# Optimization experiments

Hardware: AMD Instinct MI355X
Metric: run time of the kernel (lower is better)

## Reference

```python
import jax, jax.numpy as jnp
import numpy as np

N, E = 50000, 800000
D_IN_N, D_IN_E, D_OUT = 64, 64, 64


def setup_inputs() -> dict:
    key = jax.random.key(0)
    ks = jax.random.split(key, 10)
    stdv = 1.0 / np.sqrt(D_OUT)
    u = lambda k, shape: jax.random.uniform(k, shape, jnp.float32, -stdv, stdv)
    return {
        "nf": jax.random.normal(ks[0], (N, D_IN_N), jnp.float32),
        "ef": jax.random.normal(ks[1], (E, D_IN_E), jnp.float32),
        "src": jax.random.randint(ks[2], (E,), 0, N, jnp.int32),
        "dst": jax.random.randint(ks[3], (E,), 0, N, jnp.int32),
        "W_node": u(ks[4], (D_IN_N, D_OUT)),
        "W_edge": u(ks[5], (D_IN_E, D_OUT)),
        "bias_node": u(ks[6], (D_OUT,)),
        "bias_edge": u(ks[7], (D_OUT,)),
        "W_dense": u(ks[8], (2 * D_OUT, D_OUT)),  # Linear(2*out, out) weight, stored transposed
        "b_dense": u(ks[9], (D_OUT,)),
    }


def reference(nf, ef, src, dst, W_node, W_edge, bias_node, bias_edge, W_dense, b_dense):
    n_nodes = nf.shape[0]
    # input projections
    nf_h = nf @ W_node                     # [N, D]
    ef_h = ef @ W_edge                     # [E, D]
    # update_all: mean of incoming edge features per dst node (0 for isolated nodes, DGL default)
    deg = jax.ops.segment_sum(jnp.ones((ef_h.shape[0],), ef_h.dtype), dst, num_segments=n_nodes)
    nb_ef = jax.ops.segment_sum(ef_h, dst, num_segments=n_nodes) / jnp.maximum(deg, 1.0)[:, None]
    # apply_nodes: nf = act(nf + bias)
    nf_out = jax.nn.relu(nf_h + bias_node)
    # apply_edges (uses updated nf): cat([ef + nb_ef[dst], (nf[src]+nf[dst])/2]) -> Linear -> +bias -> act
    tmp_ef = ef_h + nb_ef[dst]             # [E, D]
    srcdst_nf = (nf_out[src] + nf_out[dst]) * 0.5
    ef_out = jnp.concatenate([tmp_ef, srcdst_nf], axis=1) @ W_dense + b_dense + bias_edge
    ef_out = jax.nn.relu(ef_out)
    return nf_out, ef_out
```

## Files before the change

### kernel.cpp

```cpp
#include <hip/hip_runtime.h>

#define D 64

typedef __attribute__((ext_vector_type(8))) short short8;
typedef __attribute__((ext_vector_type(4))) float f32x4;

__device__ __forceinline__ ushort f2b(float f) {
    union { float f; unsigned u; } x; x.f = f;
    unsigned r = x.u + 0x7FFFu + ((x.u >> 16) & 1u);
    return (ushort)(r >> 16);
}
__device__ __forceinline__ float b2f(ushort u) {
    union { float f; unsigned u; } x; x.u = ((unsigned)u) << 16;
    return x.f;
}
__device__ __forceinline__ short8 pack8(float4 a, float4 b) {
    short8 r;
    r[0] = (short)f2b(a.x); r[1] = (short)f2b(a.y); r[2] = (short)f2b(a.z); r[3] = (short)f2b(a.w);
    r[4] = (short)f2b(b.x); r[5] = (short)f2b(b.y); r[6] = (short)f2b(b.z); r[7] = (short)f2b(b.w);
    return r;
}

__global__ __launch_bounds__(256) void setup_kernel(
    const float* __restrict__ W_edge, const float* __restrict__ W_dense,
    const float* __restrict__ b_dense, const float* __restrict__ bias_edge,
    ushort* __restrict__ Wcomb_b, float* __restrict__ bias2)
{
    const int tid = threadIdx.x;
    for (int idx = tid; idx < D * D; idx += 256) {
        int k = idx >> 6, n = idx & 63;
        float s = 0.f;
        #pragma unroll 8
        for (int j = 0; j < D; ++j)
            s = fmaf(W_edge[k * D + j], W_dense[j * D + n], s);
        Wcomb_b[n * D + k] = f2b(s);
    }
    if (tid < D) bias2[tid] = b_dense[tid] + bias_edge[tid];
}

__global__ __launch_bounds__(256) void node_proj_kernel(
    const float* __restrict__ nf, const float* __restrict__ Wn,
    const float* __restrict__ bias, const float* __restrict__ Wd_bot,
    float* __restrict__ out, ushort* __restrict__ nfp_b, int N)
{
    constexpr int ROWS = 16;
    __shared__ float Ws[D * D];
    __shared__ float Wb[D * D];
    __shared__ float As[ROWS * D];
    __shared__ float Vs[ROWS * D];
    const int tid = threadIdx.x;
    const long row0 = (long)blockIdx.x * ROWS;

    #pragma unroll
    for (int i = tid; i < D * D / 4; i += 256) {
        ((float4*)Ws)[i] = ((const float4*)Wn)[i];
        float4 v = ((const float4*)Wd_bot)[i];
        ((float4*)Wb)[i] = make_float4(0.5f * v.x, 0.5f * v.y, 0.5f * v.z, 0.5f * v.w);
    }
    {
        int i = tid;
        long r = row0 + (i * 4) / D;
        ((float4*)As)[i] = (r < N) ? ((const float4*)nf)[row0 * D / 4 + i]
                                   : make_float4(0.f, 0.f, 0.f, 0.f);
    }
    __syncthreads();

    const int c = tid & 63;
    const float b = bias[c];
    for (int rr = tid >> 6; rr < ROWS; rr += 4) {
        float acc = 0.f;
        #pragma unroll
        for (int k = 0; k < D; ++k)
            acc = fmaf(As[rr * D + k], Ws[k * D + c], acc);
        float v = fmaxf(acc + b, 0.f);
        Vs[rr * D + c] = v;
        long r = row0 + rr;
        if (r < N) out[r * D + c] = v;
    }
    __syncthreads();
    for (int rr = tid >> 6; rr < ROWS; rr += 4) {
        float acc = 0.f;
        #pragma unroll
        for (int k = 0; k < D; ++k)
            acc = fmaf(Vs[rr * D + k], Wb[k * D + c], acc);
        long r = row0 + rr;
        if (r < N) nfp_b[r * D + c] = f2b(acc);
    }
}

__global__ __launch_bounds__(256) void hist_kernel(
    const int* __restrict__ dst, int* __restrict__ deg_i, int E)
{
    int i = blockIdx.x * 256 + threadIdx.x;
    if (i < E) atomicAdd(deg_i + dst[i], 1);
}

__global__ __launch_bounds__(256) void scanA_kernel(
    const int* __restrict__ deg_i, int* __restrict__ pos,
    int* __restrict__ bsum, int N)
{
    __shared__ int s[256];
    const int tid = threadIdx.x;
    const int i = blockIdx.x * 256 + tid;
    int v = (i < N) ? deg_i[i] : 0;
    s[tid] = v;
    __syncthreads();
    #pragma unroll
    for (int off = 1; off < 256; off <<= 1) {
        int t = (tid >= off) ? s[tid - off] : 0;
        __syncthreads();
        s[tid] += t;
        __syncthreads();
    }
    if (i < N) pos[i] = s[tid] - v;
    if (tid == 255) bsum[blockIdx.x] = s[255];
}

__global__ __launch_bounds__(256) void scanB_kernel(int* __restrict__ bsum, int NB)
{
    __shared__ int s[256];
    const int tid = threadIdx.x;
    int v = (tid < NB) ? bsum[tid] : 0;
    s[tid] = v;
    __syncthreads();
    #pragma unroll
    for (int off = 1; off < 256; off <<= 1) {
        int t = (tid >= off) ? s[tid - off] : 0;
        __syncthreads();
        s[tid] += t;
        __syncthreads();
    }
    if (tid < NB) bsum[tid] = s[tid] - v;
}

__global__ __launch_bounds__(256) void scanC_kernel(
    int* __restrict__ pos, int* __restrict__ cursor,
    const int* __restrict__ bsum, int N)
{
    int i = blockIdx.x * 256 + threadIdx.x;
    if (i < N) {
        int p = pos[i] + bsum[blockIdx.x];
        pos[i] = p;
        cursor[i] = p;
    }
}

__global__ __launch_bounds__(256) void scatter_kernel(
    const int* __restrict__ dst, int* __restrict__ cursor,
    int2* __restrict__ sorted_ed, int E)
{
    int i = blockIdx.x * 256 + threadIdx.x;
    if (i < E) {
        int dv = dst[i];
        int slot = atomicAdd(cursor + dv, 1);
        sorted_ed[slot] = make_int2(i, dv);
    }
}

#define SEG_ROWS 128
__global__ __launch_bounds__(256) void efp_seg_kernel(
    const float* __restrict__ ef, const int2* __restrict__ sorted_ed,
    const ushort* __restrict__ Wt, ushort* __restrict__ efp,
    float* __restrict__ nb_sum, int E)
{
    __shared__ float Sf[SEG_ROWS * 68];
    __shared__ int eids[SEG_ROWS];
    __shared__ int dsts[SEG_ROWS];
    const int tid = threadIdx.x;
    const long s0 = (long)blockIdx.x * SEG_ROWS;

    if (tid < SEG_ROWS) {
        long s = s0 + tid;
        int2 p2 = (s < E) ? sorted_ed[s] : make_int2(0, -1);
        eids[tid] = p2.x;
        dsts[tid] = p2.y;
    }
    __syncthreads();

    const int w = tid >> 6, lane = tid & 63;
    const int lr = lane & 15, g = lane >> 4;

    float4 va[2][4];
    #pragma unroll
    for (int tt = 0; tt < 2; ++tt) {
        const long erow = eids[64 * tt + 16 * w + lr];
        const float4* ap = (const float4*)(ef + erow * D);
        va[tt][0] = ap[2 * g];     va[tt][1] = ap[2 * g + 1];
        va[tt][2] = ap[8 + 2 * g]; va[tt][3] = ap[8 + 2 * g + 1];
    }

    short8 bf0[4], bf1[4];
    #pragma unroll
    for (int t = 0; t < 4; ++t) {
        bf0[t] = *(const short8*)&Wt[(16 * t + lr) * D + 8 * g];
        bf1[t] = *(const short8*)&Wt[(16 * t + lr) * D + 32 + 8 * g];
    }

    #pragma unroll
    for (int tt = 0; tt < 2; ++tt) {
        short8 a0 = pack8(va[tt][0], va[tt][1]);
        short8 a1 = pack8(va[tt][2], va[tt][3]);
        f32x4 acc[4];
        #pragma unroll
        for (int t = 0; t < 4; ++t) {
            f32x4 z = {0.f, 0.f, 0.f, 0.f};
            z = __builtin_amdgcn_mfma_f32_16x16x32_bf16(a0, bf0[t], z, 0, 0, 0);
            z = __builtin_amdgcn_mfma_f32_16x16x32_bf16(a1, bf1[t], z, 0, 0, 0);
            acc[t] = z;
        }

        #pragma unroll
        for (int t = 0; t < 4; ++t) {
            int c = 16 * t + lr;
            #pragma unroll
            for (int reg = 0; reg < 4; ++reg)
                Sf[(64 * tt + 16 * w + 4 * g + reg) * 68 + c] = acc[t][reg];
        }

        const bool odd = lane & 1;
        const int rb = 64 * tt + 16 * w + 4 * g + (odd ? 2 : 0);
        long sl0 = s0 + rb, sl1 = s0 + rb + 1;
        long eo0 = (long)eids[rb] * D, eo1 = (long)eids[rb + 1] * D;
        #pragma unroll
        for (int t = 0; t < 4; ++t) {
            float p0 = __shfl_xor(acc[t][0], 1, 64);
            float p1 = __shfl_xor(acc[t][1], 1, 64);
            float p2 = __shfl_xor(acc[t][2], 1, 64);
            float p3 = __shfl_xor(acc[t][3], 1, 64);
            float lo0, hi0, lo1, hi1;
            if (odd) { lo0 = p2; hi0 = acc[t][2]; lo1 = p3; hi1 = acc[t][3]; }
            else     { lo0 = acc[t][0]; hi0 = p0; lo1 = acc[t][1]; hi1 = p1; }
            int cbase = 16 * t + (lr & ~1);
            unsigned dw0 = ((unsigned)f2b(hi0) << 16) | (unsigned)f2b(lo0);
            unsigned dw1 = ((unsigned)f2b(hi1) << 16) | (unsigned)f2b(lo1);
            if (sl0 < E) *(unsigned*)(efp + eo0 + cbase) = dw0;
            if (sl1 < E) *(unsigned*)(efp + eo1 + cbase) = dw1;
        }
    }
    __syncthreads();

    {
        const int col = tid & 63;
        const int r0 = (tid >> 6) * 32;
        float seg = 0.f;
        int cur = dsts[r0];
        #pragma unroll 4
        for (int r = r0; r < r0 + 32; ++r) {
            int dv = dsts[r];
            if (dv != cur) {
                if (cur >= 0) atomicAdd(nb_sum + (long)cur * D + col, seg);
                seg = 0.f;
                cur = dv;
            }
            seg += Sf[r * 68 + col];
        }
        if (cur >= 0) atomicAdd(nb_sum + (long)cur * D + col, seg);
    }
}

__global__ __launch_bounds__(256) void ndp_lite_kernel(
    const float* __restrict__ nb_sum, const int* __restrict__ deg_i,
    const ushort* __restrict__ nfp_b, ushort* __restrict__ ndp_b, int N)
{
    long i = (long)blockIdx.x * 256 + threadIdx.x;
    long node = i >> 3;
    int cb = (int)(i & 7);
    if (node >= N) return;
    float inv = 1.0f / fmaxf((float)deg_i[node], 1.0f);
    const float4* sp = (const float4*)(nb_sum + node * D + cb * 8);
    float4 x0 = sp[0], x1 = sp[1];
    short8 np = *(const short8*)(nfp_b + node * D + cb * 8);
    short8 r;
    r[0] = (short)f2b(x0.x * inv + b2f((ushort)np[0]));
    r[1] = (short)f2b(x0.y * inv + b2f((ushort)np[1]));
    r[2] = (short)f2b(x0.z * inv + b2f((ushort)np[2]));
    r[3] = (short)f2b(x0.w * inv + b2f((ushort)np[3]));
    r[4] = (short)f2b(x1.x * inv + b2f((ushort)np[4]));
    r[5] = (short)f2b(x1.y * inv + b2f((ushort)np[5]));
    r[6] = (short)f2b(x1.z * inv + b2f((ushort)np[6]));
    r[7] = (short)f2b(x1.w * inv + b2f((ushort)np[7]));
    *(short8*)(ndp_b + node * D + cb * 8) = r;
}

__global__ __launch_bounds__(256) void final_kernel(
    const ushort* __restrict__ efp, const int* __restrict__ src,
    const int* __restrict__ dst, const ushort* __restrict__ ndp_b,
    const ushort* __restrict__ nfp_b, const float* __restrict__ bias2,
    float* __restrict__ out, int E)
{
    long idx = (long)blockIdx.x * 256 + threadIdx.x;
    long e = idx >> 2;
    int q = (int)(idx & 3);
    if (e >= E) return;
    int dv = dst[e], sv = src[e];
    const short8* ep = (const short8*)(efp + e * D + q * 16);
    const short8* np = (const short8*)(ndp_b + (long)dv * D + q * 16);
    const short8* sp = (const short8*)(nfp_b + (long)sv * D + q * 16);
    short8 e0 = ep[0], e1 = ep[1];
    short8 n0 = np[0], n1 = np[1];
    short8 s0 = sp[0], s1 = sp[1];
    const float4* bp = (const float4*)(bias2 + q * 16);
    float4 b0 = bp[0], b1 = bp[1], b2 = bp[2], b3 = bp[3];

    float r[16];
    #pragma unroll
    for (int j = 0; j < 8; ++j) {
        r[j]     = b2f((ushort)e0[j]) + b2f((ushort)n0[j]) + b2f((ushort)s0[j]);
        r[8 + j] = b2f((ushort)e1[j]) + b2f((ushort)n1[j]) + b2f((ushort)s1[j]);
    }
    float4* op = (float4*)(out + e * D + q * 16);
    op[0] = make_float4(fmaxf(r[0] + b0.x, 0.f), fmaxf(r[1] + b0.y, 0.f),
                        fmaxf(r[2] + b0.z, 0.f), fmaxf(r[3] + b0.w, 0.f));
    op[1] = make_float4(fmaxf(r[4] + b1.x, 0.f), fmaxf(r[5] + b1.y, 0.f),
                        fmaxf(r[6] + b1.z, 0.f), fmaxf(r[7] + b1.w, 0.f));
    op[2] = make_float4(fmaxf(r[8] + b2.x, 0.f), fmaxf(r[9] + b2.y, 0.f),
                        fmaxf(r[10] + b2.z, 0.f), fmaxf(r[11] + b2.w, 0.f));
    op[3] = make_float4(fmaxf(r[12] + b3.x, 0.f), fmaxf(r[13] + b3.y, 0.f),
                        fmaxf(r[14] + b3.z, 0.f), fmaxf(r[15] + b3.w, 0.f));
}

extern "C" void kernel_launch(void* const* d_in, const int* in_sizes, int n_in,
                              void* d_out, int out_size, void* d_ws, size_t ws_size,
                              hipStream_t stream) {
    const float* nf        = (const float*)d_in[0];
    const float* ef        = (const float*)d_in[1];
    const int*   src       = (const int*)d_in[2];
    const int*   dst       = (const int*)d_in[3];
    const float* W_node    = (const float*)d_in[4];
    const float* W_edge    = (const float*)d_in[5];
    const float* bias_node = (const float*)d_in[6];
    const float* bias_edge = (const float*)d_in[7];
    const float* W_dense   = (const float*)d_in[8];
    const float* b_dense   = (const float*)d_in[9];

    const int N = in_sizes[0] / D;
    const int E = in_sizes[1] / D;
    const int NB = (N + 255) / 256;

    float* nf_out = (float*)d_out;
    float* ef_out = (float*)d_out + (size_t)N * D;

    char* p = (char*)d_ws;
    int*    deg_i    = (int*)p;     p += (size_t)N * 4;
    float*  nb_sum   = (float*)p;   p += (size_t)N * D * 4;
    size_t  zbytes   = (size_t)(p - (char*)d_ws);
    int*    pos      = (int*)p;     p += (size_t)N * 4;
    int*    cursor   = (int*)p;     p += (size_t)N * 4;
    int*    bsum     = (int*)p;     p += 256 * 4;
    int2*   sorted_ed= (int2*)p;    p += (size_t)E * 8;
    ushort* nfp_b    = (ushort*)p;  p += (size_t)N * D * 2;
    ushort* ndp_b    = (ushort*)p;  p += (size_t)N * D * 2;
    ushort* Wcomb_b  = (ushort*)p;  p += D * D * 2;
    float*  bias2    = (float*)p;   p += 256;
    ushort* efp      = (ushort*)p;

    hipMemsetAsync(d_ws, 0, zbytes, stream);

    setup_kernel<<<1, 256, 0, stream>>>(W_edge, W_dense, b_dense, bias_edge,
                                        Wcomb_b, bias2);
    node_proj_kernel<<<(N + 15) / 16, 256, 0, stream>>>(nf, W_node, bias_node,
                                                        W_dense + D * D, nf_out, nfp_b, N);
    hist_kernel<<<(E + 255) / 256, 256, 0, stream>>>(dst, deg_i, E);
    scanA_kernel<<<NB, 256, 0, stream>>>(deg_i, pos, bsum, N);
    scanB_kernel<<<1, 256, 0, stream>>>(bsum, NB);
    scanC_kernel<<<NB, 256, 0, stream>>>(pos, cursor, bsum, N);
    scatter_kernel<<<(E + 255) / 256, 256, 0, stream>>>(dst, cursor, sorted_ed, E);
    efp_seg_kernel<<<(E + SEG_ROWS - 1) / SEG_ROWS, 256, 0, stream>>>(
        ef, sorted_ed, Wcomb_b, efp, nb_sum, E);
    ndp_lite_kernel<<<(int)(((size_t)N * 8 + 255) / 256), 256, 0, stream>>>(
        nb_sum, deg_i, nfp_b, ndp_b, N);
    final_kernel<<<(int)(((size_t)E * 4 + 255) / 256), 256, 0, stream>>>(
        efp, src, dst, ndp_b, nfp_b, bias2, ef_out, E);
}
```

Baseline: 392.2 us.

## Load edge ids directly, stage bf16 results in LDS, trim scan writes

The segment kernel now reads sorted edge ids straight from global memory into registers instead of first staging them in shared memory behind a barrier. This lets the gathers of edge features start earlier. Projected results are kept in LDS as packed bf16 pairs, which halves LDS footprint and traffic, and the segmented reduction now runs over 16-row chunks with two columns per thread. scanC no longer writes pos back. The risk is that summing bf16-rounded values changes nb_sum precision, and 16-row chunks may issue more atomics.

```diff
diff --git a/kernel.cpp b/kernel.cpp
--- a/kernel.cpp
+++ b/kernel.cpp
@@ -134,15 +134,11 @@
 }
 
 __global__ __launch_bounds__(256) void scanC_kernel(
-    int* __restrict__ pos, int* __restrict__ cursor,
+    const int* __restrict__ pos, int* __restrict__ cursor,
     const int* __restrict__ bsum, int N)
 {
     int i = blockIdx.x * 256 + threadIdx.x;
-    if (i < N) {
-        int p = pos[i] + bsum[blockIdx.x];
-        pos[i] = p;
-        cursor[i] = p;
-    }
+    if (i < N) cursor[i] = pos[i] + bsum[blockIdx.x];
 }
 
 __global__ __launch_bounds__(256) void scatter_kernel(
@@ -163,30 +159,42 @@
     const ushort* __restrict__ Wt, ushort* __restrict__ efp,
     float* __restrict__ nb_sum, int E)
 {
-    __shared__ float Sf[SEG_ROWS * 68];
-    __shared__ int eids[SEG_ROWS];
+    __shared__ unsigned Slds[SEG_ROWS * 33];
     __shared__ int dsts[SEG_ROWS];
     const int tid = threadIdx.x;
     const long s0 = (long)blockIdx.x * SEG_ROWS;
 
+    const int w = tid >> 6, lane = tid & 63;
+    const int lr = lane & 15, g = lane >> 4;
+    const bool odd = lane & 1;
+
+    long gde[2];
+    #pragma unroll
+    for (int tt = 0; tt < 2; ++tt) {
+        long s = s0 + 64 * tt + 16 * w + lr;
+        if (s >= E) s = E - 1;
+        gde[tt] = (long)sorted_ed[s].x;
+    }
+    float4 va[2][4];
+    #pragma unroll
+    for (int tt = 0; tt < 2; ++tt) {
+        const float4* ap = (const float4*)(ef + gde[tt] * D);
+        va[tt][0] = ap[2 * g];     va[tt][1] = ap[2 * g + 1];
+        va[tt][2] = ap[8 + 2 * g]; va[tt][3] = ap[8 + 2 * g + 1];
+    }
+    int rbl[2]; long seo[2][2];
+    #pragma unroll
+    for (int tt = 0; tt < 2; ++tt) {
+        rbl[tt] = 64 * tt + 16 * w + 4 * g + (odd ? 2 : 0);
+        long s = s0 + rbl[tt];
+        if (s > E - 2) s = (E - 2) & ~1L;
+        int4 q = *(const int4*)&sorted_ed[s];
+        seo[tt][0] = (long)q.x * D;
+        seo[tt][1] = (long)q.z * D;
+    }
     if (tid < SEG_ROWS) {
         long s = s0 + tid;
-        int2 p2 = (s < E) ? sorted_ed[s] : make_int2(0, -1);
-        eids[tid] = p2.x;
-        dsts[tid] = p2.y;
-    }
-    __syncthreads();
-
-    const int w = tid >> 6, lane = tid & 63;
-    const int lr = lane & 15, g = lane >> 4;
-
-    float4 va[2][4];
-    #pragma unroll
-    for (int tt = 0; tt < 2; ++tt) {
-        const long erow = eids[64 * tt + 16 * w + lr];
-        const float4* ap = (const float4*)(ef + erow * D);
-        va[tt][0] = ap[2 * g];     va[tt][1] = ap[2 * g + 1];
-        va[tt][2] = ap[8 + 2 * g]; va[tt][3] = ap[8 + 2 * g + 1];
+        dsts[tid] = (s < E) ? sorted_ed[s].y : -1;
     }
 
     short8 bf0[4], bf1[4];
@@ -209,18 +217,8 @@
             acc[t] = z;
         }
 
-        #pragma unroll
-        for (int t = 0; t < 4; ++t) {
-            int c = 16 * t + lr;
-            #pragma unroll
-            for (int reg = 0; reg < 4; ++reg)
-                Sf[(64 * tt + 16 * w + 4 * g + reg) * 68 + c] = acc[t][reg];
-        }
-
-        const bool odd = lane & 1;
-        const int rb = 64 * tt + 16 * w + 4 * g + (odd ? 2 : 0);
+        const int rb = rbl[tt];
         long sl0 = s0 + rb, sl1 = s0 + rb + 1;
-        long eo0 = (long)eids[rb] * D, eo1 = (long)eids[rb + 1] * D;
         #pragma unroll
         for (int t = 0; t < 4; ++t) {
             float p0 = __shfl_xor(acc[t][0], 1, 64);
@@ -231,30 +229,41 @@
             if (odd) { lo0 = p2; hi0 = acc[t][2]; lo1 = p3; hi1 = acc[t][3]; }
             else     { lo0 = acc[t][0]; hi0 = p0; lo1 = acc[t][1]; hi1 = p1; }
             int cbase = 16 * t + (lr & ~1);
+            int dc = cbase >> 1;
             unsigned dw0 = ((unsigned)f2b(hi0) << 16) | (unsigned)f2b(lo0);
             unsigned dw1 = ((unsigned)f2b(hi1) << 16) | (unsigned)f2b(lo1);
-            if (sl0 < E) *(unsigned*)(efp + eo0 + cbase) = dw0;
-            if (sl1 < E) *(unsigned*)(efp + eo1 + cbase) = dw1;
+            if (sl0 < E) *(unsigned*)(efp + seo[tt][0] + cbase) = dw0;
+            if (sl1 < E) *(unsigned*)(efp + seo[tt][1] + cbase) = dw1;
+            Slds[rb * 33 + dc]       = dw0;
+            Slds[(rb + 1) * 33 + dc] = dw1;
         }
     }
     __syncthreads();
 
     {
-        const int col = tid & 63;
-        const int r0 = (tid >> 6) * 32;
-        float seg = 0.f;
+        const int dwc = tid & 31;
+        const int r0 = (tid >> 5) * 16;
+        float seg0 = 0.f, seg1 = 0.f;
         int cur = dsts[r0];
         #pragma unroll 4
-        for (int r = r0; r < r0 + 32; ++r) {
+        for (int r = r0; r < r0 + 16; ++r) {
             int dv = dsts[r];
+            unsigned u = Slds[r * 33 + dwc];
             if (dv != cur) {
-                if (cur >= 0) atomicAdd(nb_sum + (long)cur * D + col, seg);
-                seg = 0.f;
+                if (cur >= 0) {
+                    atomicAdd(nb_sum + (long)cur * D + 2 * dwc, seg0);
+                    atomicAdd(nb_sum + (long)cur * D + 2 * dwc + 1, seg1);
+                }
+                seg0 = seg1 = 0.f;
                 cur = dv;
             }
-            seg += Sf[r * 68 + col];
+            seg0 += b2f((ushort)(u & 0xffff));
+            seg1 += b2f((ushort)(u >> 16));
         }
-        if (cur >= 0) atomicAdd(nb_sum + (long)cur * D + col, seg);
+        if (cur >= 0) {
+            atomicAdd(nb_sum + (long)cur * D + 2 * dwc, seg0);
+            atomicAdd(nb_sum + (long)cur * D + 2 * dwc + 1, seg1);
+        }
     }
 }
 
```

Result: no change. 399.5 us (median of 2 runs) (+1.9%).
